# Performance work log

Measured on AMD Instinct MI355X. Metric: run time of the kernel, lower is better.

Reference implementation:

```python
import jax, jax.numpy as jnp
import numpy as np

E = 384      # hidden_dim
H = 8        # num_attention_heads
D = E // H   # head_dim = 48


def setup_inputs() -> dict:
    key = jax.random.key(0)
    ks = jax.random.split(key, 11)
    B, S = 4, 2048
    patch_embeds = jax.random.normal(ks[0], (B, S, E), dtype=jnp.float32)
    attention_mask = jax.random.randint(ks[1], (B, S), 0, 2).astype(bool)
    s = 1.0 / np.sqrt(E)
    Wq = jax.random.normal(ks[2], (E, E), dtype=jnp.float32) * s
    bq = jnp.zeros((E,), dtype=jnp.float32)
    Wk = jax.random.normal(ks[3], (E, E), dtype=jnp.float32) * s
    bk = jnp.zeros((E,), dtype=jnp.float32)
    Wv = jax.random.normal(ks[4], (E, E), dtype=jnp.float32) * s
    bv = jnp.zeros((E,), dtype=jnp.float32)
    Wo = jax.random.normal(ks[5], (E, E), dtype=jnp.float32) * s
    bo = jnp.zeros((E,), dtype=jnp.float32)
    return {"patch_embeds": patch_embeds, "attention_mask": attention_mask,
            "Wq": Wq, "bq": bq, "Wk": Wk, "bk": bk,
            "Wv": Wv, "bv": bv, "Wo": Wo, "bo": bo}


def reference(patch_embeds, attention_mask, Wq, bq, Wk, bk, Wv, bv, Wo, bo):
    B, S, _ = patch_embeds.shape
    scale = D ** (-0.5)
    # QKV projections (nn.Linear: x @ W.T + b); W stored as [out,in]
    q = patch_embeds @ Wq.T + bq
    k = patch_embeds @ Wk.T + bk
    v = patch_embeds @ Wv.T + bv
    # [B,S,E] -> [B,H,S,D]
    q = q.reshape(B, S, H, D).transpose(0, 2, 1, 3)
    k = k.reshape(B, S, H, D).transpose(0, 2, 1, 3)
    v = v.reshape(B, S, H, D).transpose(0, 2, 1, 3)
    # scaled dot-product attention with key mask (True = masked)
    scores = jnp.einsum('bhqd,bhkd->bhqk', q, k) * scale
    mask = attention_mask[:, None, None, :]  # [B,1,1,S]
    scores = jnp.where(mask, -jnp.inf, scores)
    weights = jax.nn.softmax(scores, axis=-1)
    out = jnp.einsum('bhqk,bhkd->bhqd', weights, v)
    out = out.transpose(0, 2, 1, 3).reshape(B, S, E)
    return out @ Wo.T + bo
```

## Files before the change

kernel.cpp:

```cpp
#include <hip/hip_runtime.h>
#include <math.h>

#define B_ 4
#define S_ 2048
#define E_ 384
#define H_ 8
#define D_ 48
#define M_ (B_*S_)
#define DP_ 64
constexpr float QK_SCALE = 0.14433756729740643f * 1.4426950408889634f;

typedef __attribute__((ext_vector_type(8))) short short8;
typedef __attribute__((ext_vector_type(4))) float f32x4;
typedef unsigned short u16;

__device__ inline u16 f2bf(float f) {
    unsigned u = __float_as_uint(f);
    return (u16)((u + 0x7FFFu + ((u >> 16) & 1u)) >> 16);
}
__device__ inline float bf2f(u16 h) { return __uint_as_float(((unsigned)h) << 16); }
__device__ inline unsigned pk2(float a, float b) {
    return (unsigned)f2bf(a) | ((unsigned)f2bf(b) << 16);
}
__device__ inline unsigned pk2_fast(float a, float b) {
#if __has_builtin(__builtin_amdgcn_perm)
    unsigned ua = __float_as_uint(a) + 0x8000u;
    unsigned ub = __float_as_uint(b) + 0x8000u;
    return __builtin_amdgcn_perm(ub, ua, 0x07060302u);
#else
    return pk2(a, b);
#endif
}
__device__ inline float fexp2(float x) {
#if __has_builtin(__builtin_amdgcn_exp2f)
    return __builtin_amdgcn_exp2f(x);
#else
    return exp2f(x);
#endif
}
__device__ inline void glld16(const void* g, void* l) {
    __builtin_amdgcn_global_load_lds((const __attribute__((address_space(1))) unsigned int*)g,
                                     (__attribute__((address_space(3))) unsigned int*)l, 16, 0, 0);
}

__global__ __launch_bounds__(256) void prep(const float4* __restrict__ x,
                                            const int* __restrict__ mask,
                                            const float4* __restrict__ wq,
                                            const float4* __restrict__ wk,
                                            const float4* __restrict__ wv,
                                            const float4* __restrict__ wo,
                                            uint2* __restrict__ xb,
                                            uint2* __restrict__ wb,
                                            u16* __restrict__ Qp, u16* __restrict__ Kp) {
    const int bx = blockIdx.x, t = threadIdx.x;
    if (bx < 3072) {
        int i = bx * 256 + t;
        float4 v = x[i];
        uint2 H;
        H.x = pk2(v.x, v.y);
        H.y = pk2(v.z, v.w);
        xb[i] = H;
    } else if (bx < 3072 + 144) {
        int i = (bx - 3072) * 256 + t;
        const int n4 = 36864;
        const float4* srcs[4] = {wq, wk, wv, wo};
        #pragma unroll
        for (int j = 0; j < 4; ++j) {
            float4 v = srcs[j][i];
            uint2 H;
            H.x = pk2(v.x, v.y);
            H.y = pk2(v.z, v.w);
            wb[(size_t)j * n4 + i] = H;
        }
    } else {
        int i = (bx - 3216) * 256 + t;
        int bh = i >> 11, s = i & 2047, b = bh >> 3;
        size_t off = ((size_t)bh * S_ + s) * DP_ + 48;
        uint4 qz = {0x00004300u, 0, 0, 0};
        uint4 kz = {mask[b * S_ + s] ? 0x0000BF80u : 0u, 0, 0, 0};
        uint4 z  = {0, 0, 0, 0};
        *reinterpret_cast<uint4*>(Qp + off)     = qz;
        *reinterpret_cast<uint4*>(Qp + off + 8) = z;
        *reinterpret_cast<uint4*>(Kp + off)     = kz;
        *reinterpret_cast<uint4*>(Kp + off + 8) = z;
    }
}

template <int MT>
__device__ __forceinline__ void gemm_core(const u16* __restrict__ ab,
                                          const u16* __restrict__ wbp,
                                          int m0, int n0, f32x4 acc[MT][4],
                                          u16* As, u16* Ws) {
    const int t = threadIdx.x, w = t >> 6, lane = t & 63;
    const int ln = lane & 15, quad = lane >> 4;
    const int gr = lane >> 3;
    const int gc = (lane & 7) ^ gr;

    #pragma unroll
    for (int mt = 0; mt < MT; ++mt)
        #pragma unroll
        for (int nt = 0; nt < 4; ++nt)
            acc[mt][nt] = (f32x4){0.f, 0.f, 0.f, 0.f};

    for (int kk = 0; kk < 384; kk += 64) {
        __syncthreads();
        #pragma unroll
        for (int i = 0; i < 2 * MT; ++i) {
            int r0 = w * (16 * MT) + i * 8;
            size_t goff = (size_t)(m0 + r0 + gr) * E_ + kk + gc * 8;
            glld16(ab + goff, As + r0 * 64);
        }
        #pragma unroll
        for (int i = 0; i < 2; ++i) {
            int r0 = w * 16 + i * 8;
            size_t goff = (size_t)(n0 + r0 + gr) * E_ + kk + gc * 8;
            glld16(wbp + goff, Ws + r0 * 64);
        }
        __syncthreads();

        #pragma unroll
        for (int ks = 0; ks < 2; ++ks) {
            const int slot = (ks * 4 + quad) ^ (ln & 7);
            short8 ah[MT], wfh[4];
            #pragma unroll
            for (int mt = 0; mt < MT; ++mt) {
                int row = w * (16 * MT) + mt * 16 + ln;
                ah[mt] = *reinterpret_cast<const short8*>(&As[row * 64 + slot * 8]);
            }
            #pragma unroll
            for (int nt = 0; nt < 4; ++nt) {
                int row = nt * 16 + ln;
                wfh[nt] = *reinterpret_cast<const short8*>(&Ws[row * 64 + slot * 8]);
            }
            #pragma unroll
            for (int mt = 0; mt < MT; ++mt)
                #pragma unroll
                for (int nt = 0; nt < 4; ++nt)
                    acc[mt][nt] = __builtin_amdgcn_mfma_f32_16x16x32_bf16(ah[mt], wfh[nt], acc[mt][nt], 0, 0, 0);
        }
    }
}

__global__ __launch_bounds__(256) void gemm_qkv(const u16* __restrict__ xb,
                                                const u16* __restrict__ wb,
                                                const float* __restrict__ bq, const float* __restrict__ bk,
                                                const float* __restrict__ bv,
                                                u16* __restrict__ Qp, u16* __restrict__ Kp,
                                                u16* __restrict__ Vtp) {
    __shared__ u16 smem[128 * 64 + 64 * 64];
    u16* As = smem;
    u16* Ws = smem + 128 * 64;

    const int y = blockIdx.y;
    const int wsel = y / 6;
    const int n0 = (y - wsel * 6) * 64;
    const int m0 = blockIdx.x * 128;
    const u16* wh = wb + (size_t)wsel * 147456;

    f32x4 acc[2][4];
    gemm_core<2>(xb, wh, m0, n0, acc, As, Ws);

    const int t = threadIdx.x, w = t >> 6, lane = t & 63;
    const int ln = lane & 15, quad = lane >> 4;
    const int b  = m0 >> 11;
    const float* bias = (wsel == 0) ? bq : (wsel == 1) ? bk : bv;

    if (wsel == 2) {
        const int s_base = (m0 & 2047) + w * 32 + quad * 4;
        #pragma unroll
        for (int nt = 0; nt < 4; ++nt) {
            const int col = n0 + nt * 16 + ln;
            const int h   = (col * 683) >> 15;
            const int d   = col - h * 48;
            const float bc = bias[col];
            u16* dst = Vtp + ((size_t)(b * 8 + h) * 48 + d) * 2048;
            #pragma unroll
            for (int mt = 0; mt < 2; ++mt) {
                int s0 = s_base + mt * 16;
                uint2 pk;
                pk.x = pk2(acc[mt][nt][0] + bc, acc[mt][nt][1] + bc);
                pk.y = pk2(acc[mt][nt][2] + bc, acc[mt][nt][3] + bc);
                *reinterpret_cast<uint2*>(dst + s0) = pk;
            }
        }
    } else {
        const float scale = (wsel == 0) ? QK_SCALE : 1.0f;
        u16* Tr = smem;
        __syncthreads();
        #pragma unroll
        for (int nt = 0; nt < 4; ++nt) {
            const float bc = bias[n0 + nt * 16 + ln];
            #pragma unroll
            for (int mt = 0; mt < 2; ++mt)
                #pragma unroll
                for (int r = 0; r < 4; ++r) {
                    int row = w * 32 + mt * 16 + quad * 4 + r;
                    Tr[row * 76 + nt * 16 + ln] = f2bf((acc[mt][nt][r] + bc) * scale);
                }
        }
        __syncthreads();
        const int row  = t >> 1, half = t & 1;
        const int s    = (m0 & 2047) + row;
        const u16* src = &Tr[row * 76 + half * 32];
        u16* base = (wsel == 0) ? Qp : Kp;
        #pragma unroll
        for (int c = 0; c < 4; ++c) {
            int gcol = n0 + half * 32 + c * 8;
            int h = (gcol * 683) >> 15;
            int d = gcol - h * 48;
            u16* dst = base + ((size_t)(b * 8 + h) * 2048 + s) * DP_ + d;
            *reinterpret_cast<uint4*>(dst) = *reinterpret_cast<const uint4*>(src + c * 8);
        }
    }
}

__global__ __launch_bounds__(256) void gemm_out(const u16* __restrict__ ab,
                                                const u16* __restrict__ wb,
                                                const float* __restrict__ bo, float* __restrict__ out) {
    __shared__ u16 smem[64 * 64 + 64 * 64];
    u16* As = smem;
    u16* Ws = smem + 64 * 64;
    const int m0 = blockIdx.x * 64, n0 = blockIdx.y * 64;
    const u16* wh = wb + (size_t)3 * 147456;
    f32x4 acc[1][4];
    gemm_core<1>(ab, wh, m0, n0, acc, As, Ws);

    const int t = threadIdx.x, w = t >> 6, lane = t & 63;
    const int ln = lane & 15, quad = lane >> 4;
    #pragma unroll
    for (int nt = 0; nt < 4; ++nt) {
        const int col = n0 + nt * 16 + ln;
        const float bc = bo[col];
        #pragma unroll
        for (int r = 0; r < 4; ++r) {
            size_t row = (size_t)(m0 + w * 16 + quad * 4 + r);
            out[row * E_ + col] = acc[0][nt][r] + bc;
        }
    }
}

__global__ __launch_bounds__(256, 2) void attn_mfma(const u16* __restrict__ Qp,
                                                    const u16* __restrict__ Kp,
                                                    const u16* __restrict__ Vtp,
                                                    u16* __restrict__ AO) {
    __shared__ __align__(16) u16 QPs[128 * 64];
    __shared__ __align__(16) u16 Ksh[2][64 * 64];
    __shared__ __align__(16) u16 Vt[2][48 * 64];
    __shared__ float linv[4][32];

    const int t    = threadIdx.x;
    const int w    = t >> 6;
    const int lane = t & 63;
    const int ln   = lane & 15;
    const int quad = lane >> 4;
    const int gr   = lane >> 3;
    const int gc   = (lane & 7) ^ gr;
    const int q0   = blockIdx.x * 128;
    const int bh   = blockIdx.y;
    const int b    = bh >> 3, h = bh & 7;
    const int cb   = h * 48;
    const size_t rb = (size_t)b * S_;

    const u16* Qsrc = Qp  + ((size_t)bh * S_ + q0) * DP_;
    const u16* Ksrc = Kp  + (size_t)bh * S_ * DP_;
    const u16* Vsrc = Vtp + (size_t)bh * 48 * 2048;

    const int swz0 = ((quad    ) ^ (ln & 7)) << 3;
    const int swz1 = ((4 + quad) ^ (ln & 7)) << 3;
    const u16* kA[2][2], *vA[2][2];
    #pragma unroll
    for (int bf = 0; bf < 2; ++bf) {
        kA[bf][0] = &Ksh[bf][ln * 64 + swz0];
        kA[bf][1] = &Ksh[bf][ln * 64 + swz1];
        vA[bf][0] = &Vt[bf][ln * 64 + swz0];
        vA[bf][1] = &Vt[bf][ln * 64 + swz1];
    }
    int qrow[2];
    const u16 *pR[2][2];
    u16* pW[2][4];
    #pragma unroll
    for (int qt = 0; qt < 2; ++qt) {
        qrow[qt] = (w * 32 + qt * 16 + ln) * 64;
        pR[qt][0] = &QPs[qrow[qt] + swz0];
        pR[qt][1] = &QPs[qrow[qt] + swz1];
        #pragma unroll
        for (int Mt = 0; Mt < 4; ++Mt)
            pW[qt][Mt] = &QPs[qrow[qt] +
                ((((Mt * 2 + (quad >> 1)) ^ (ln & 7)) << 3) | ((quad & 1) << 2))];
    }

    auto stage = [&](int bf, int kt) {
        const int k0 = kt * 64;
        glld16(Ksrc + (size_t)(k0 + w * 16 + gr) * DP_ + gc * 8,     &Ksh[bf][(w * 16) * 64]);
        glld16(Ksrc + (size_t)(k0 + w * 16 + 8 + gr) * DP_ + gc * 8, &Ksh[bf][(w * 16 + 8) * 64]);
        if (w < 3) {
            glld16(Vsrc + (size_t)(w * 16 + gr) * 2048 + k0 + gc * 8,     &Vt[bf][(w * 16) * 64]);
            glld16(Vsrc + (size_t)(w * 16 + 8 + gr) * 2048 + k0 + gc * 8, &Vt[bf][(w * 16 + 8) * 64]);
        }
    };

    #pragma unroll
    for (int i = 0; i < 4; ++i) {
        int r0 = w * 32 + i * 8;
        glld16(Qsrc + (size_t)(r0 + gr) * DP_ + gc * 8, &QPs[r0 * 64]);
    }
    stage(0, 0);
    __syncthreads();

    short8 qf[2][2];
    #pragma unroll
    for (int qt = 0; qt < 2; ++qt) {
        qf[qt][0] = *reinterpret_cast<const short8*>(pR[qt][0]);
        qf[qt][1] = *reinterpret_cast<const short8*>(pR[qt][1]);
    }

    f32x4 o[2][3];
    #pragma unroll
    for (int qt = 0; qt < 2; ++qt)
        #pragma unroll
        for (int nt = 0; nt < 3; ++nt) o[qt][nt] = (f32x4){0.f, 0.f, 0.f, 0.f};
    float lq[2] = {0.f, 0.f};

    auto body = [&](int cur, int nxt, int ktn) {
        if (ktn < 32) stage(nxt, ktn);

        f32x4 sc[4][2];
        #pragma unroll
        for (int Mt = 0; Mt < 4; ++Mt) {
            short8 kf0 = *reinterpret_cast<const short8*>(kA[cur][0] + Mt * 1024);
            short8 kf1 = *reinterpret_cast<const short8*>(kA[cur][1] + Mt * 1024);
            #pragma unroll
            for (int qt = 0; qt < 2; ++qt) {
                f32x4 a0 = __builtin_amdgcn_mfma_f32_16x16x32_bf16(kf0, qf[qt][0], (f32x4){0.f,0.f,0.f,0.f}, 0, 0, 0);
                sc[Mt][qt] = __builtin_amdgcn_mfma_f32_16x16x32_bf16(kf1, qf[qt][1], a0, 0, 0, 0);
            }
        }

        #pragma unroll
        for (int qt = 0; qt < 2; ++qt)
            #pragma unroll
            for (int Mt = 0; Mt < 4; ++Mt) {
                float p0 = fexp2(sc[Mt][qt][0]);
                float p1 = fexp2(sc[Mt][qt][1]);
                float p2 = fexp2(sc[Mt][qt][2]);
                float p3 = fexp2(sc[Mt][qt][3]);
                lq[qt] += (p0 + p1) + (p2 + p3);
                uint2 pk;
                pk.x = pk2_fast(p0, p1);
                pk.y = pk2_fast(p2, p3);
                *reinterpret_cast<uint2*>(pW[qt][Mt]) = pk;
            }

        short8 pa[2][2];
        #pragma unroll
        for (int qt = 0; qt < 2; ++qt) {
            pa[qt][0] = *reinterpret_cast<const short8*>(pR[qt][0]);
            pa[qt][1] = *reinterpret_cast<const short8*>(pR[qt][1]);
        }
        #pragma unroll
        for (int nt = 0; nt < 3; ++nt) {
            short8 vb0 = *reinterpret_cast<const short8*>(vA[cur][0] + nt * 1024);
            short8 vb1 = *reinterpret_cast<const short8*>(vA[cur][1] + nt * 1024);
            #pragma unroll
            for (int qt = 0; qt < 2; ++qt) {
                o[qt][nt] = __builtin_amdgcn_mfma_f32_16x16x32_bf16(pa[qt][0], vb0, o[qt][nt], 0, 0, 0);
                o[qt][nt] = __builtin_amdgcn_mfma_f32_16x16x32_bf16(pa[qt][1], vb1, o[qt][nt], 0, 0, 0);
            }
        }
        __syncthreads();
    };

    for (int kt = 0; kt < 32; kt += 2) {
        body(0, 1, kt + 1);
        body(1, 0, kt + 2);
    }

    #pragma unroll
    for (int qt = 0; qt < 2; ++qt) {
        float l = lq[qt];
        l += __shfl_xor(l, 16);
        l += __shfl_xor(l, 32);
        if (quad == 0) linv[w][qt * 16 + ln] = 1.0f / l;
    }
    __syncthreads();
    #pragma unroll
    for (int qt = 0; qt < 2; ++qt) {
        f32x4 il = *reinterpret_cast<const f32x4*>(&linv[w][qt * 16 + quad * 4]);
        #pragma unroll
        for (int nt = 0; nt < 3; ++nt)
            #pragma unroll
            for (int r = 0; r < 4; ++r) {
                size_t row = rb + q0 + w * 32 + qt * 16 + quad * 4 + r;
                size_t idx = row * E_ + cb + nt * 16 + ln;
                AO[idx] = f2bf(o[qt][nt][r] * il[r]);
            }
    }
}

extern "C" void kernel_launch(void* const* d_in, const int* in_sizes, int n_in,
                              void* d_out, int out_size, void* d_ws, size_t ws_size,
                              hipStream_t stream) {
    (void)in_sizes; (void)n_in; (void)out_size; (void)ws_size;
    const float* x    = (const float*)d_in[0];
    const int*   mask = (const int*)  d_in[1];
    const float* Wq   = (const float*)d_in[2];
    const float* bq   = (const float*)d_in[3];
    const float* Wk   = (const float*)d_in[4];
    const float* bk   = (const float*)d_in[5];
    const float* Wv   = (const float*)d_in[6];
    const float* bv   = (const float*)d_in[7];
    const float* Wo   = (const float*)d_in[8];
    const float* bo   = (const float*)d_in[9];

    const size_t NELEM = (size_t)M_ * E_;
    const size_t WELEM = (size_t)E_ * E_;
    const size_t PEL   = (size_t)B_ * H_ * S_ * DP_;
    u16* ws = (u16*)d_ws;
    u16* xb  = ws;
    u16* wb  = xb + NELEM;
    u16* Qp  = wb + 4 * WELEM;
    u16* Kp  = Qp + PEL;
    u16* Vtp = Kp + PEL;
    u16* AO  = xb;

    dim3 blk(256);
    prep<<<dim3(3472), blk, 0, stream>>>(
        (const float4*)x, mask,
        (const float4*)Wq, (const float4*)Wk, (const float4*)Wv, (const float4*)Wo,
        (uint2*)xb, (uint2*)wb, Qp, Kp);

    gemm_qkv<<<dim3(M_ / 128, 18), blk, 0, stream>>>(xb, wb, bq, bk, bv, Qp, Kp, Vtp);

    attn_mfma<<<dim3(S_ / 128, B_ * H_), blk, 0, stream>>>(Qp, Kp, Vtp, AO);

    gemm_out<<<dim3(M_ / 64, 6), blk, 0, stream>>>(AO, wb, bo, (float*)d_out);
}
```

Before: 152.8 us.

## Double-buffer GEMM shared-memory tiles and swap attention grid axes

The shared GEMM core now uses two LDS buffers, issuing the next K-slice's global-to-LDS loads before computing on the current slice, with one barrier per iteration instead of two. LDS allocations in both GEMM kernels double to hold the ping-pong buffers. The attention launch also swaps its grid axes so consecutive blocks cover different batch-heads rather than consecutive query tiles, which changes scheduling order and cache locality. The larger LDS footprint may lower occupancy. Overlap also depends on the async load helper not waiting before compute.

```diff
diff --git a/kernel.cpp b/kernel.cpp
--- a/kernel.cpp
+++ b/kernel.cpp
@@ -102,22 +102,30 @@
         for (int nt = 0; nt < 4; ++nt)
             acc[mt][nt] = (f32x4){0.f, 0.f, 0.f, 0.f};
 
-    for (int kk = 0; kk < 384; kk += 64) {
-        __syncthreads();
+    auto stage = [&](int bf, int kk) {
+        u16* Ab = As + bf * (MT * 4096);
+        u16* Wb = Ws + bf * 4096;
         #pragma unroll
         for (int i = 0; i < 2 * MT; ++i) {
             int r0 = w * (16 * MT) + i * 8;
-            size_t goff = (size_t)(m0 + r0 + gr) * E_ + kk + gc * 8;
-            glld16(ab + goff, As + r0 * 64);
+            glld16(ab + (size_t)(m0 + r0 + gr) * E_ + kk + gc * 8, Ab + r0 * 64);
         }
         #pragma unroll
         for (int i = 0; i < 2; ++i) {
             int r0 = w * 16 + i * 8;
-            size_t goff = (size_t)(n0 + r0 + gr) * E_ + kk + gc * 8;
-            glld16(wbp + goff, Ws + r0 * 64);
-        }
-        __syncthreads();
-
+            glld16(wbp + (size_t)(n0 + r0 + gr) * E_ + kk + gc * 8, Wb + r0 * 64);
+        }
+    };
+
+    stage(0, 0);
+    __syncthreads();
+
+    #pragma unroll
+    for (int it = 0; it < 6; ++it) {
+        const int cur = it & 1;
+        if (it < 5) stage(cur ^ 1, (it + 1) * 64);
+        const u16* Ab = As + cur * (MT * 4096);
+        const u16* Wb = Ws + cur * 4096;
         #pragma unroll
         for (int ks = 0; ks < 2; ++ks) {
             const int slot = (ks * 4 + quad) ^ (ln & 7);
@@ -125,12 +133,12 @@
             #pragma unroll
             for (int mt = 0; mt < MT; ++mt) {
                 int row = w * (16 * MT) + mt * 16 + ln;
-                ah[mt] = *reinterpret_cast<const short8*>(&As[row * 64 + slot * 8]);
+                ah[mt] = *reinterpret_cast<const short8*>(&Ab[row * 64 + slot * 8]);
             }
             #pragma unroll
             for (int nt = 0; nt < 4; ++nt) {
                 int row = nt * 16 + ln;
-                wfh[nt] = *reinterpret_cast<const short8*>(&Ws[row * 64 + slot * 8]);
+                wfh[nt] = *reinterpret_cast<const short8*>(&Wb[row * 64 + slot * 8]);
             }
             #pragma unroll
             for (int mt = 0; mt < MT; ++mt)
@@ -138,6 +146,7 @@
                 for (int nt = 0; nt < 4; ++nt)
                     acc[mt][nt] = __builtin_amdgcn_mfma_f32_16x16x32_bf16(ah[mt], wfh[nt], acc[mt][nt], 0, 0, 0);
         }
+        __syncthreads();
     }
 }
 
@@ -147,9 +156,9 @@
                                                 const float* __restrict__ bv,
                                                 u16* __restrict__ Qp, u16* __restrict__ Kp,
                                                 u16* __restrict__ Vtp) {
-    __shared__ u16 smem[128 * 64 + 64 * 64];
+    __shared__ u16 smem[2 * 2 * 4096 + 2 * 4096];
     u16* As = smem;
-    u16* Ws = smem + 128 * 64;
+    u16* Ws = smem + 2 * 2 * 4096;
 
     const int y = blockIdx.y;
     const int wsel = y / 6;
@@ -217,9 +226,9 @@
 __global__ __launch_bounds__(256) void gemm_out(const u16* __restrict__ ab,
                                                 const u16* __restrict__ wb,
                                                 const float* __restrict__ bo, float* __restrict__ out) {
-    __shared__ u16 smem[64 * 64 + 64 * 64];
+    __shared__ u16 smem[2 * 4096 + 2 * 4096];
     u16* As = smem;
-    u16* Ws = smem + 64 * 64;
+    u16* Ws = smem + 2 * 4096;
     const int m0 = blockIdx.x * 64, n0 = blockIdx.y * 64;
     const u16* wh = wb + (size_t)3 * 147456;
     f32x4 acc[1][4];
@@ -255,8 +264,8 @@
     const int quad = lane >> 4;
     const int gr   = lane >> 3;
     const int gc   = (lane & 7) ^ gr;
-    const int q0   = blockIdx.x * 128;
-    const int bh   = blockIdx.y;
+    const int bh   = blockIdx.x;
+    const int q0   = blockIdx.y * 128;
     const int b    = bh >> 3, h = bh & 7;
     const int cb   = h * 48;
     const size_t rb = (size_t)b * S_;
@@ -431,7 +440,7 @@
 
     gemm_qkv<<<dim3(M_ / 128, 18), blk, 0, stream>>>(xb, wb, bq, bk, bv, Qp, Kp, Vtp);
 
-    attn_mfma<<<dim3(S_ / 128, B_ * H_), blk, 0, stream>>>(Qp, Kp, Vtp, AO);
+    attn_mfma<<<dim3(B_ * H_, S_ / 128), blk, 0, stream>>>(Qp, Kp, Vtp, AO);
 
     gemm_out<<<dim3(M_ / 64, 6), blk, 0, stream>>>(AO, wb, bo, (float*)d_out);
 }
```

New measurement: 148.3 us. -2.9%, faster.
